# Kernel optimization log

Measured on AMD Instinct MI355X. Metric: run time of the kernel, lower is better.

The kernel has to match this reference:

```python
import jax, jax.numpy as jnp
import numpy as np

N_TOKENS = 8192
IN_F = 4096
OUT_F = 4096
QMIN, QMAX = -128, 127  # get_quantized_range(8)
IN_SCALE = 0.02
OUT_SCALE = 0.05
IN_ZP = 0
OUT_ZP = 0


def setup_inputs() -> dict:
    key = jax.random.key(0)
    k1, k2, k3, k4 = jax.random.split(key, 4)
    x = jax.random.randint(k1, (N_TOKENS, IN_F), QMIN, QMAX + 1, dtype=jnp.int8)
    weight = jax.random.randint(k2, (OUT_F, IN_F), QMIN, QMAX + 1, dtype=jnp.int8)
    bias = jax.random.randint(k3, (OUT_F,), -1000, 1001, dtype=jnp.int32)
    weight_scale = jax.random.uniform(k4, (OUT_F, 1), dtype=jnp.float32, minval=0.005, maxval=0.02)
    return {"x": x, "weight": weight, "bias": bias, "weight_scale": weight_scale}


def reference(x, weight, bias, weight_scale):
    # int32-accumulated GEMM: [N, in] @ [in, out] + bias  (CPU path of the torch module)
    acc = jnp.matmul(x.astype(jnp.int32), weight.T.astype(jnp.int32)) + bias  # [N, out] int32
    ws = jnp.swapaxes(weight_scale, -1, -2)  # [1, out] per-output-channel scale
    out = acc.astype(jnp.float32) * (IN_SCALE * ws / OUT_SCALE)
    out = out + OUT_ZP
    out = jnp.clip(jnp.round(out), QMIN, QMAX).astype(jnp.int8)
    return out
```

## Files before the change

kernel.cpp:

```cpp
#include <hip/hip_runtime.h>
#include <hip/hip_bf16.h>
#include <stdint.h>

#define N_TOKENS 8192
#define IN_F 4096
#define OUT_F 4096

#define BM 128
#define BN 128
#define BK 64
#define KITERS (IN_F / BK)

typedef int int32x4 __attribute__((ext_vector_type(4)));

__device__ __forceinline__ void gload_lds16(const void* g, void* lds) {
  __builtin_amdgcn_global_load_lds(
      (const __attribute__((address_space(1))) void*)g,
      (__attribute__((address_space(3))) void*)lds, 16, 0, 0);
}

__global__ void pack_kernel(const int4* __restrict__ xs, const int4* __restrict__ ws,
                            uchar4* __restrict__ xd, uchar4* __restrict__ wd,
                            int n4x, int n4tot) {
  const int stride = gridDim.x * blockDim.x;
  for (int i = blockIdx.x * blockDim.x + threadIdx.x; i < n4tot; i += stride) {
    int4 v;
    if (i < n4x) v = xs[i];
    else v = ws[i - n4x];
    uchar4 p;
    p.x = (unsigned char)(v.x & 255);
    p.y = (unsigned char)(v.y & 255);
    p.z = (unsigned char)(v.z & 255);
    p.w = (unsigned char)(v.w & 255);
    if (i < n4x) xd[i] = p;
    else wd[i - n4x] = p;
  }
}

__global__ __launch_bounds__(256) void gemm_i8(
    const signed char* __restrict__ A, const signed char* __restrict__ B,
    const int* __restrict__ bias, const float* __restrict__ wscale,
    int* __restrict__ out) {
  __shared__ signed char sA[BM * BK];
  __shared__ signed char sB[BN * BK];

  const int tid = threadIdx.x;
  const int lane = tid & 63;
  const int wid = tid >> 6;
  const int wr = wid >> 1;
  const int wc = wid & 1;

  const int bid = blockIdx.x;
  const int swz = (bid & 7) * 256 + (bid >> 3);
  const int brow = (swz >> 5) * BM;
  const int bcol = (swz & 31) * BN;

  const int srow = tid >> 2;
  const int schunk = tid & 3;

  int32x4 acc[4][4];
#pragma unroll
  for (int m = 0; m < 4; ++m)
#pragma unroll
    for (int n = 0; n < 4; ++n) acc[m][n] = (int32x4){0, 0, 0, 0};

  for (int kt = 0; kt < KITERS; ++kt) {
    const int k0 = kt * BK;
#pragma unroll
    for (int h = 0; h < 2; ++h) {
      int row = h * 64 + srow;
      int sc = schunk ^ ((row >> 1) & 3);
      gload_lds16(A + (size_t)(brow + row) * IN_F + k0 + sc * 16,
                  &sA[row * BK + schunk * 16]);
      gload_lds16(B + (size_t)(bcol + row) * IN_F + k0 + sc * 16,
                  &sB[row * BK + schunk * 16]);
    }
    __syncthreads();

    int32x4 af[4], bf[4];
#pragma unroll
    for (int m = 0; m < 4; ++m) {
      int row = wr * 64 + m * 16 + (lane & 15);
      int ch = (lane >> 4) ^ ((row >> 1) & 3);
      af[m] = *(const int32x4*)&sA[row * BK + ch * 16];
    }
#pragma unroll
    for (int n = 0; n < 4; ++n) {
      int row = wc * 64 + n * 16 + (lane & 15);
      int ch = (lane >> 4) ^ ((row >> 1) & 3);
      bf[n] = *(const int32x4*)&sB[row * BK + ch * 16];
    }
#pragma unroll
    for (int m = 0; m < 4; ++m)
#pragma unroll
      for (int n = 0; n < 4; ++n)
        acc[m][n] =
            __builtin_amdgcn_mfma_i32_16x16x64_i8(af[m], bf[n], acc[m][n], 0, 0, 0);
    __syncthreads();
  }

  const int col_b = bcol + wc * 64 + (lane & 15);
  const int row_b = brow + wr * 64 + ((lane >> 4) << 2);
#pragma unroll
  for (int n = 0; n < 4; ++n) {
    int col = col_b + n * 16;
    float s = 0.02f * wscale[col] / 0.05f;
    int bz = bias[col];
#pragma unroll
    for (int m = 0; m < 4; ++m) {
      int row0 = row_b + m * 16;
#pragma unroll
      for (int r = 0; r < 4; ++r) {
        float f = (float)(acc[m][n][r] + bz) * s;
        f = rintf(f);
        f = fminf(127.f, fmaxf(-128.f, f));
        out[(size_t)(row0 + r) * OUT_F + col] = (int)f;
      }
    }
  }
}

extern "C" void kernel_launch(void* const* d_in, const int* in_sizes, int n_in,
                              void* d_out, int out_size, void* d_ws, size_t ws_size,
                              hipStream_t stream) {
  const int* x = (const int*)d_in[0];
  const int* w = (const int*)d_in[1];
  const int* bias = (const int*)d_in[2];
  const float* wsc = (const float*)d_in[3];
  int* out = (int*)d_out;

  signed char* xp = (signed char*)d_ws;
  signed char* wp = xp + (size_t)N_TOKENS * IN_F;

  const int n4x = N_TOKENS * IN_F / 4;
  const int n4w = OUT_F * IN_F / 4;
  const int n4tot = n4x + n4w;

  pack_kernel<<<2048, 256, 0, stream>>>((const int4*)x, (const int4*)w,
                                        (uchar4*)xp, (uchar4*)wp, n4x, n4tot);

  gemm_i8<<<2048, 256, 0, stream>>>(xp, wp, bias, wsc, out);
}
```

Before: 439.2 us.

## Use 256x256 tiles with triple-buffered LDS pipeline and 8 waves

```diff
diff --git a/kernel.cpp b/kernel.cpp
--- a/kernel.cpp
+++ b/kernel.cpp
@@ -6,14 +6,14 @@
 #define IN_F 4096
 #define OUT_F 4096
 
-#define BM 128
-#define BN 128
-#define BK 64
-#define KITERS (IN_F / BK)
+#define BM 256
+#define BN 256
+#define BKB 64
+#define NKT (IN_F / BKB)
 
 typedef int int32x4 __attribute__((ext_vector_type(4)));
 
-__device__ __forceinline__ void gload_lds16(const void* g, void* lds) {
+__device__ __forceinline__ void gload_lds16(const signed char* g, signed char* lds) {
   __builtin_amdgcn_global_load_lds(
       (const __attribute__((address_space(1))) void*)g,
       (__attribute__((address_space(3))) void*)lds, 16, 0, 0);
@@ -37,78 +37,101 @@
   }
 }
 
-__global__ __launch_bounds__(256) void gemm_i8(
+__global__ __launch_bounds__(512, 2) void gemm_i8(
     const signed char* __restrict__ A, const signed char* __restrict__ B,
     const int* __restrict__ bias, const float* __restrict__ wscale,
     int* __restrict__ out) {
-  __shared__ signed char sA[BM * BK];
-  __shared__ signed char sB[BN * BK];
+  __shared__ __align__(16) signed char sA[3][BM * BKB];
+  __shared__ __align__(16) signed char sB[3][BN * BKB];
 
   const int tid = threadIdx.x;
   const int lane = tid & 63;
-  const int wid = tid >> 6;
-  const int wr = wid >> 1;
-  const int wc = wid & 1;
+  const int w = tid >> 6;
+  const int wr = w >> 2;
+  const int wc = w & 3;
 
-  const int bid = blockIdx.x;
-  const int swz = (bid & 7) * 256 + (bid >> 3);
-  const int brow = (swz >> 5) * BM;
-  const int bcol = (swz & 31) * BN;
+  const int brow = blockIdx.y * BM;
+  const int bcol = blockIdx.x * BN;
 
-  const int srow = tid >> 2;
-  const int schunk = tid & 3;
+  const int csrc = (((lane & 3) ^ ((lane >> 3) & 3)) << 4);
+  const int r0 = w * 16 + (lane >> 2);
+  const signed char* gA0 = A + (size_t)(brow + r0) * IN_F + csrc;
+  const signed char* gB0 = B + (size_t)(bcol + r0) * IN_F + csrc;
+  const int ldst = w * 1024 + lane * 16;
 
-  int32x4 acc[4][4];
+#define STAGE(tt, bf)                                                  \
+  do {                                                                 \
+    const size_t ko = (size_t)(tt)*BKB;                                \
+    gload_lds16(gA0 + ko, &sA[bf][ldst]);                              \
+    gload_lds16(gA0 + ko + (size_t)128 * IN_F, &sA[bf][ldst + 8192]);  \
+    gload_lds16(gB0 + ko, &sB[bf][ldst]);                              \
+    gload_lds16(gB0 + ko + (size_t)128 * IN_F, &sB[bf][ldst + 8192]);  \
+  } while (0)
+
+  const int cfrag = (((lane >> 4) ^ ((lane >> 1) & 3)) << 4);
+  const int aoff = (wr * 128 + (lane & 15)) * BKB + cfrag;
+  const int boff = (wc * 64 + (lane & 15)) * BKB + cfrag;
+
+  int32x4 acc[8][4];
 #pragma unroll
-  for (int m = 0; m < 4; ++m)
+  for (int m = 0; m < 8; ++m)
 #pragma unroll
     for (int n = 0; n < 4; ++n) acc[m][n] = (int32x4){0, 0, 0, 0};
 
-  for (int kt = 0; kt < KITERS; ++kt) {
-    const int k0 = kt * BK;
+  STAGE(0, 0);
+  STAGE(1, 1);
+  asm volatile("s_waitcnt vmcnt(4)" ::: "memory");
+  __builtin_amdgcn_s_barrier();
+
+  int bufR = 0, bufS = 2;
+  for (int t = 0; t < NKT; ++t) {
+    if (t < NKT - 2) STAGE(t + 2, bufS);
+
+    int32x4 a[8], b[4];
 #pragma unroll
-    for (int h = 0; h < 2; ++h) {
-      int row = h * 64 + srow;
-      int sc = schunk ^ ((row >> 1) & 3);
-      gload_lds16(A + (size_t)(brow + row) * IN_F + k0 + sc * 16,
-                  &sA[row * BK + schunk * 16]);
-      gload_lds16(B + (size_t)(bcol + row) * IN_F + k0 + sc * 16,
-                  &sB[row * BK + schunk * 16]);
-    }
-    __syncthreads();
-
-    int32x4 af[4], bf[4];
+    for (int n = 0; n < 4; ++n) b[n] = *(const int32x4*)&sB[bufR][boff + n * 1024];
 #pragma unroll
-    for (int m = 0; m < 4; ++m) {
-      int row = wr * 64 + m * 16 + (lane & 15);
-      int ch = (lane >> 4) ^ ((row >> 1) & 3);
-      af[m] = *(const int32x4*)&sA[row * BK + ch * 16];
-    }
-#pragma unroll
-    for (int n = 0; n < 4; ++n) {
-      int row = wc * 64 + n * 16 + (lane & 15);
-      int ch = (lane >> 4) ^ ((row >> 1) & 3);
-      bf[n] = *(const int32x4*)&sB[row * BK + ch * 16];
-    }
+    for (int m = 0; m < 4; ++m) a[m] = *(const int32x4*)&sA[bufR][aoff + m * 1024];
+    __builtin_amdgcn_s_setprio(1);
 #pragma unroll
     for (int m = 0; m < 4; ++m)
 #pragma unroll
       for (int n = 0; n < 4; ++n)
-        acc[m][n] =
-            __builtin_amdgcn_mfma_i32_16x16x64_i8(af[m], bf[n], acc[m][n], 0, 0, 0);
-    __syncthreads();
+        acc[m][n] = __builtin_amdgcn_mfma_i32_16x16x64_i8(a[m], b[n], acc[m][n], 0, 0, 0);
+    __builtin_amdgcn_s_setprio(0);
+    __builtin_amdgcn_s_barrier();
+#pragma unroll
+    for (int m = 4; m < 8; ++m) a[m] = *(const int32x4*)&sA[bufR][aoff + m * 1024];
+    __builtin_amdgcn_s_setprio(1);
+#pragma unroll
+    for (int m = 4; m < 8; ++m)
+#pragma unroll
+      for (int n = 0; n < 4; ++n)
+        acc[m][n] = __builtin_amdgcn_mfma_i32_16x16x64_i8(a[m], b[n], acc[m][n], 0, 0, 0);
+    __builtin_amdgcn_s_setprio(0);
+
+    if (t < NKT - 2) {
+      asm volatile("s_waitcnt vmcnt(4) lgkmcnt(0)" ::: "memory");
+      __builtin_amdgcn_s_barrier();
+    } else if (t == NKT - 2) {
+      asm volatile("s_waitcnt vmcnt(0) lgkmcnt(0)" ::: "memory");
+      __builtin_amdgcn_s_barrier();
+    }
+    bufR = (bufR == 2) ? 0 : bufR + 1;
+    bufS = (bufS == 2) ? 0 : bufS + 1;
   }
+#undef STAGE
 
-  const int col_b = bcol + wc * 64 + (lane & 15);
-  const int row_b = brow + wr * 64 + ((lane >> 4) << 2);
+  const int colb = bcol + wc * 64 + (lane & 15);
+  const int rowb = brow + wr * 128 + ((lane >> 4) << 2);
 #pragma unroll
   for (int n = 0; n < 4; ++n) {
-    int col = col_b + n * 16;
-    float s = 0.02f * wscale[col] / 0.05f;
-    int bz = bias[col];
+    const int col = colb + n * 16;
+    const float s = 0.02f * wscale[col] / 0.05f;
+    const int bz = bias[col];
 #pragma unroll
-    for (int m = 0; m < 4; ++m) {
-      int row0 = row_b + m * 16;
+    for (int m = 0; m < 8; ++m) {
+      const int row0 = rowb + m * 16;
 #pragma unroll
       for (int r = 0; r < 4; ++r) {
         float f = (float)(acc[m][n][r] + bz) * s;
@@ -139,5 +162,6 @@
   pack_kernel<<<2048, 256, 0, stream>>>((const int4*)x, (const int4*)w,
                                         (uchar4*)xp, (uchar4*)wp, n4x, n4tot);
 
-  gemm_i8<<<2048, 256, 0, stream>>>(xp, wp, bias, wsc, out);
+  dim3 grid(OUT_F / BN, N_TOKENS / BM);
+  gemm_i8<<<grid, dim3(512), 0, stream>>>(xp, wp, bias, wsc, out);
 }
```

Result: no change. 442.0 us (+0.6%).
